# Performance work log

Measured on AMD Instinct MI355X. Metric: run time of the kernel, lower is better.

## Reference

```python
import jax, jax.numpy as jnp
import numpy as np

K = 10  # CSLS neighborhood size


def setup_inputs() -> dict:
    key = jax.random.key(0)
    k1, k2 = jax.random.split(key)
    N, D = 16384, 512
    Lvec = jax.random.normal(k1, (N, D), dtype=jnp.float32)
    Rvec = jax.random.normal(k2, (N, D), dtype=jnp.float32)
    return {"Lvec": Lvec, "Rvec": Rvec}


def reference(Lvec, Rvec):
    N = Lvec.shape[0]
    # L_sim[i, j] = <L_i, R_j>; R_sim = L_sim.T since both slices cover all rows
    sim = jnp.matmul(Lvec, Rvec.T)                      # [N_L, N_R]
    # CSLS penalties: mean of top-k similarities per row
    LR = jnp.mean(jax.lax.top_k(sim, K)[0], axis=-1)    # [N_L] per-L-entity top-k avg
    RL = jnp.mean(jax.lax.top_k(sim.T, K)[0], axis=-1)  # [N_R] per-R-entity top-k avg
    # Faithful to the torch epoch-0 broadcasting: both penalties broadcast over columns
    # csls[i, j] = 2 * R_sim[i, j] - LR[j] - RL[j]
    csls = 2.0 * sim.T - LR[None, :] - RL[None, :]      # [N_R, N_L]
    order = jnp.argsort(-csls, axis=-1)                 # descending rank lists
    # rank position of the true answer (column i for row i)
    ranks = jnp.argmax(order == jnp.arange(N)[:, None], axis=-1)  # [N] int
    top1_val = jnp.max(csls, axis=-1)                   # top-1 CSLS score per row
    return (ranks.astype(jnp.int32), top1_val)
```

## Files before the change

kernel.cpp:

```cpp
#include <hip/hip_runtime.h>
#include <hip/hip_bf16.h>
#include <hip/hip_fp8.h>
#include <stdint.h>

#define NN 16384
#define DD 512
#define BM 128
#define BN 256
#define NCT2 64
#define KT 6
#define EPW 264
#define NEG_INF (-3.0e38f)


typedef unsigned short u16;
typedef _Float16 f16;
typedef __attribute__((ext_vector_type(8))) __bf16 bf16x8;
typedef __attribute__((ext_vector_type(8))) short sh8;
typedef __attribute__((ext_vector_type(8))) _Float16 f16x8;
typedef __attribute__((ext_vector_type(4))) float f32x4;

__device__ __forceinline__ u16 f2bf(float f) {
  uint32_t x = __float_as_uint(f);
  x += 0x7fffu + ((x >> 16) & 1u);
  return (u16)(x >> 16);
}
__device__ __forceinline__ float bf2f(u16 u) {
  return __uint_as_float(((uint32_t)u) << 16);
}
__device__ __forceinline__ float f16bits(uint32_t bits) {
  f16 h;
  u16 b = (u16)bits;
  __builtin_memcpy(&h, &b, 2);
  return (float)h;
}
__device__ __forceinline__ u16 h2bits(f16 h) {
  u16 b;
  __builtin_memcpy(&b, &h, 2);
  return b;
}
__device__ __forceinline__ uint8_t f2fp8(float f) {
  __hip_fp8_e4m3 h(f);
  return (uint8_t)h.__x;
}
__device__ __forceinline__ float fp82f(uint8_t b) {
  __hip_fp8_e4m3 h;
  h.__x = (__hip_fp8_storage_t)b;
  return (float)h;
}
__device__ __forceinline__ uint32_t pk_max16(uint32_t a, uint32_t b) {
  uint32_t d;
  asm("v_pk_max_f16 %0, %1, %2" : "=v"(d) : "v"(a), "v"(b));
  return d;
}
__device__ __forceinline__ uint32_t pk_min16(uint32_t a, uint32_t b) {
  uint32_t d;
  asm("v_pk_min_f16 %0, %1, %2" : "=v"(d) : "v"(a), "v"(b));
  return d;
}

__device__ __forceinline__ void gload_lds16(const u16* g, u16* lds) {
  __builtin_amdgcn_global_load_lds(
      (const __attribute__((address_space(1))) uint32_t*)g,
      (__attribute__((address_space(3))) uint32_t*)lds,
      16, 0, 0);
}

template <int N>
__device__ __forceinline__ void insN(float (&t)[N], float v) {
  #pragma unroll
  for (int j = 0; j < N; ++j) {
    float hi = fmaxf(t[j], v);
    v = fminf(t[j], v);
    t[j] = hi;
  }
}
template <int N>
__device__ __forceinline__ void pinsN(uint32_t (&t)[N], uint32_t v) {
  #pragma unroll
  for (int j = 0; j < N; ++j) {
    uint32_t hi = pk_max16(t[j], v);
    v = pk_min16(t[j], v);
    t[j] = hi;
  }
}

__global__ __launch_bounds__(256) void cast_kernel(const float* __restrict__ src,
                                                   u16* __restrict__ dst) {
  int i = (blockIdx.x * 256 + threadIdx.x) * 8;
  const float4* s4 = reinterpret_cast<const float4*>(src + i);
  float4 a = s4[0], b = s4[1];
  sh8 o;
  o[0] = (short)f2bf(a.x); o[1] = (short)f2bf(a.y);
  o[2] = (short)f2bf(a.z); o[3] = (short)f2bf(a.w);
  o[4] = (short)f2bf(b.x); o[5] = (short)f2bf(b.y);
  o[6] = (short)f2bf(b.z); o[7] = (short)f2bf(b.w);
  *reinterpret_cast<sh8*>(dst + i) = o;
}

__global__ __launch_bounds__(256) void diag_kernel(const u16* __restrict__ Lb,
                                                   const u16* __restrict__ Rb,
                                                   float* __restrict__ diag) {
  int r = blockIdx.x * 4 + (threadIdx.x >> 6);
  int lane = threadIdx.x & 63;
  sh8 a = *reinterpret_cast<const sh8*>(Lb + (size_t)r * DD + lane * 8);
  sh8 b = *reinterpret_cast<const sh8*>(Rb + (size_t)r * DD + lane * 8);
  float s = 0.f;
  #pragma unroll
  for (int j = 0; j < 8; ++j) s += bf2f((u16)a[j]) * bf2f((u16)b[j]);
  #pragma unroll
  for (int off = 32; off > 0; off >>= 1) s += __shfl_down(s, off);
  if (lane == 0) diag[r] = s;
}

#define DECODE_TILE(ct0)                                \
  const int xcd = blockIdx.x & 7;                       \
  const int idx = blockIdx.x >> 3;                      \
  const int rowtile = xcd * 16 + (idx & 15);            \
  const int coltile = (ct0) + (idx >> 4);               \
  const int rowbase = rowtile * BM;                     \
  const int colbase = coltile * BN;                     \
  const int tid = threadIdx.x;                          \
  const int w = tid >> 6;                               \
  const int lane = tid & 63;                            \
  const int quad = lane >> 4;                           \
  const int l16 = lane & 15;                            \
  const int wr = (w >> 2) * 64;                         \
  const int wc = (w & 3) * 64;                          \
  (void)xcd; (void)lane;

#define GEMM_PRE()                                                              \
  const int rp0_ = tid >> 3, gp0_ = (tid & 7) ^ (rp0_ & 7);                     \
  const int grow0_ = rp0_ * 2 + (gp0_ >> 2), gcol0_ = (gp0_ & 3) * 8;           \
  const int gl1_ = tid + 512;                                                   \
  const int rp1_ = gl1_ >> 3, gp1_ = (gl1_ & 7) ^ (rp1_ & 7);                   \
  const int grow1_ = rp1_ * 2 + (gp1_ >> 2), gcol1_ = (gp1_ & 3) * 8;           \
  const u16* gA_  = A + (size_t)(rowbase + grow0_) * DD + gcol0_;               \
  const u16* gB0_ = B + (size_t)(colbase + grow0_) * DD + gcol0_;               \
  const u16* gB1_ = B + (size_t)(colbase + grow1_) * DD + gcol1_;               \
  const int gsel_ = ((((l16) & 1) << 2) + quad) ^ (l16 >> 1);                   \
  const int rdA_ = (wr / 2 + (l16 >> 1)) * 64 + gsel_ * 8;                      \
  const int rdB_ = (wc / 2 + (l16 >> 1)) * 64 + gsel_ * 8;

#define STAGE(t, dA, dB)                                                        \
  gload_lds16(gA_  + (t) * 32, (dA) + tid * 8);                                 \
  gload_lds16(gB0_ + (t) * 32, (dB) + tid * 8);                                 \
  gload_lds16(gB1_ + (t) * 32, (dB) + 4096 + tid * 8);

#define GEMM_K_LOOP(sA0_, sA1_, sB0_, sB1_)                                     \
  f32x4 acc[4][4];                                                              \
  _Pragma("unroll")                                                             \
  for (int a_ = 0; a_ < 4; ++a_)                                                \
    _Pragma("unroll")                                                           \
    for (int b_ = 0; b_ < 4; ++b_) acc[a_][b_] = (f32x4){0.f, 0.f, 0.f, 0.f};   \
  {                                                                             \
    GEMM_PRE()                                                                  \
    u16* const bufA_[2] = {(sA0_), (sA1_)};                                     \
    u16* const bufB_[2] = {(sB0_), (sB1_)};                                     \
    STAGE(0, bufA_[0], bufB_[0])                                                \
    STAGE(1, bufA_[1], bufB_[1])                                                \
    _Pragma("unroll")                                                           \
    for (int t = 0; t < 16; ++t) {                                              \
      if (t < 15) { asm volatile("s_waitcnt vmcnt(3)" ::: "memory"); }          \
      else        { asm volatile("s_waitcnt vmcnt(0)" ::: "memory"); }          \
      __builtin_amdgcn_s_barrier();                                             \
      asm volatile("" ::: "memory");                                            \
      {                                                                         \
        const u16* cA_ = bufA_[t & 1];                                          \
        const u16* cB_ = bufB_[t & 1];                                          \
        bf16x8 af[4], bfv[4];                                                   \
        _Pragma("unroll")                                                       \
        for (int f = 0; f < 4; ++f)                                             \
          af[f]  = *reinterpret_cast<const bf16x8*>(cA_ + rdA_ + f * 512);      \
        _Pragma("unroll")                                                       \
        for (int f = 0; f < 4; ++f)                                             \
          bfv[f] = *reinterpret_cast<const bf16x8*>(cB_ + rdB_ + f * 512);      \
        _Pragma("unroll")                                                       \
        for (int fr = 0; fr < 4; ++fr)                                          \
          _Pragma("unroll")                                                     \
          for (int fc = 0; fc < 4; ++fc)                                        \
            acc[fr][fc] = __builtin_amdgcn_mfma_f32_16x16x32_bf16(af[fr], bfv[fc], acc[fr][fc], 0, 0, 0); \
      }                                                                         \
      asm volatile("" ::: "memory");                                            \
      __builtin_amdgcn_s_barrier();                                             \
      if (t + 2 < 16) { STAGE(t + 2, bufA_[t & 1], bufB_[t & 1]) }              \
    }                                                                           \
  }

__global__ __launch_bounds__(512, 4) void gemm_topk(const u16* __restrict__ A,
                                                    const u16* __restrict__ B,
                                                    f16* __restrict__ rowp,
                                                    f16* __restrict__ colp,
                                                    uint8_t* __restrict__ sim,
                                                    int SC2) {
  __shared__ __align__(16) u16 smem[33792];
  u16* sA0 = smem;
  u16* sA1 = smem + 4096;
  u16* sB0 = smem + 8192;
  u16* sB1 = smem + 16384;
  DECODE_TILE(0)
  GEMM_K_LOOP(sA0, sA1, sB0, sB1)

  f16* hC = reinterpret_cast<f16*>(smem);
  #pragma unroll
  for (int fr = 0; fr < 4; ++fr)
    #pragma unroll
    for (int fc = 0; fc < 4; ++fc)
      #pragma unroll
      for (int reg = 0; reg < 4; ++reg)
        hC[(wr + 16 * fr + quad * 4 + reg) * EPW + wc + 16 * fc + l16] =
            (f16)acc[fr][fc][reg];
  __syncthreads();
  if (coltile < SC2) {
    const int SW = SC2 * BN;
    uint8_t* gs = sim + (size_t)rowbase * SW + (size_t)coltile * BN;
    #pragma unroll
    for (int itw = 0; itw < 8; ++itw) {
      int idx2 = itw * 4096 + tid * 8;
      int rr = idx2 >> 8, cc = idx2 & 255;
      f16x8 v = *reinterpret_cast<const f16x8*>(hC + rr * EPW + cc);
      uint32_t lo = 0, hi = 0;
      #pragma unroll
      for (int j = 0; j < 4; ++j) lo |= (uint32_t)f2fp8((float)v[j]) << (8 * j);
      #pragma unroll
      for (int j = 0; j < 4; ++j) hi |= (uint32_t)f2fp8((float)v[4 + j]) << (8 * j);
      uint2 o;
      o.x = lo; o.y = hi;
      *reinterpret_cast<uint2*>(gs + (size_t)rr * SW + cc) = o;
    }
  }
  uint32_t trow[KT];
  #pragma unroll
  for (int j = 0; j < KT; ++j) trow[j] = 0xFBFFFBFFu;
  {
    const u16* q = reinterpret_cast<const u16*>(hC) + (tid >> 2) * EPW + (tid & 3) * 64;
    #pragma unroll
    for (int c8 = 0; c8 < 8; ++c8) {
      uint4 ch = *reinterpret_cast<const uint4*>(q + c8 * 8);
      pinsN<KT>(trow, ch.x);
      pinsN<KT>(trow, ch.y);
      pinsN<KT>(trow, ch.z);
      pinsN<KT>(trow, ch.w);
    }
  }
  uint32_t tcol[KT];
  #pragma unroll
  for (int j = 0; j < KT; ++j) tcol[j] = 0xFBFFFBFFu;
  const int cp = tid & 127, rq = tid >> 7;
  {
    const u16* base = reinterpret_cast<const u16*>(hC) + rq * 32 * EPW + 2 * cp;
    #pragma unroll 8
    for (int i = 0; i < 32; ++i) {
      uint32_t v = *reinterpret_cast<const uint32_t*>(base + i * EPW);
      pinsN<KT>(tcol, v);
    }
  }
  __syncthreads();
  uint32_t* sCl = reinterpret_cast<uint32_t*>(smem);
  uint32_t* sRl = reinterpret_cast<uint32_t*>(smem) + 128 * 4 * KT;
  #pragma unroll
  for (int j = 0; j < KT; ++j) sCl[(cp * 4 + rq) * KT + j] = tcol[j];
  #pragma unroll
  for (int j = 0; j < KT; ++j) sRl[tid * KT + j] = trow[j];
  __syncthreads();
  if (tid < 256) {
    float best[KT];
    #pragma unroll
    for (int j = 0; j < KT; ++j) best[j] = NEG_INF;
    const int cpp = tid >> 1, par = tid & 1;
    for (int rqi = 0; rqi < 4; ++rqi)
      for (int j = 0; j < KT; ++j) {
        uint32_t u = sCl[(cpp * 4 + rqi) * KT + j];
        float v = f16bits(par ? (u >> 16) : u);
        if (v > best[KT - 1]) insN<KT>(best, v);
        else break;
      }
    f16* o = colp + ((size_t)rowtile * NN + colbase + tid) * KT;
    uint32_t w0 = h2bits((f16)best[0]) | ((uint32_t)h2bits((f16)best[1]) << 16);
    uint32_t w1 = h2bits((f16)best[2]) | ((uint32_t)h2bits((f16)best[3]) << 16);
    uint32_t w2 = h2bits((f16)best[4]) | ((uint32_t)h2bits((f16)best[5]) << 16);
    uint32_t* o32 = reinterpret_cast<uint32_t*>(o);
    o32[0] = w0; o32[1] = w1; o32[2] = w2;
  } else if (tid < 384) {
    const int r = tid - 256;
    float best[KT];
    #pragma unroll
    for (int j = 0; j < KT; ++j) best[j] = NEG_INF;
    for (int h = 0; h < 4; ++h)
      for (int par = 0; par < 2; ++par)
        for (int j = 0; j < KT; ++j) {
          uint32_t u = sRl[(r * 4 + h) * KT + j];
          float v = f16bits(par ? (u >> 16) : u);
          if (v > best[KT - 1]) insN<KT>(best, v);
          else break;
        }
    f16* o = rowp + ((size_t)coltile * NN + rowbase + r) * KT;
    uint32_t w0 = h2bits((f16)best[0]) | ((uint32_t)h2bits((f16)best[1]) << 16);
    uint32_t w1 = h2bits((f16)best[2]) | ((uint32_t)h2bits((f16)best[3]) << 16);
    uint32_t w2 = h2bits((f16)best[4]) | ((uint32_t)h2bits((f16)best[5]) << 16);
    uint32_t* o32 = reinterpret_cast<uint32_t*>(o);
    o32[0] = w0; o32[1] = w1; o32[2] = w2;
  }
}

__global__ __launch_bounds__(512, 4) void gemm_rank(const u16* __restrict__ A,
                                                    const u16* __restrict__ B,
                                                    const float* __restrict__ p,
                                                    const float* __restrict__ thr,
                                                    int* __restrict__ cnt_out,
                                                    float* __restrict__ mx_out,
                                                    int ct0) {
  __shared__ __align__(16) u16 smem[24576];
  u16* sA0 = smem;
  u16* sA1 = smem + 4096;
  u16* sB0 = smem + 8192;
  u16* sB1 = smem + 16384;
  DECODE_TILE(ct0)

  GEMM_K_LOOP(sA0, sA1, sB0, sB1)

  float thrv[16];
  #pragma unroll
  for (int i = 0; i < 16; ++i)
    thrv[i] = thr[rowbase + wr + 16 * (i >> 2) + quad * 4 + (i & 3)];
  float pv[4];
  #pragma unroll
  for (int fc = 0; fc < 4; ++fc) pv[fc] = p[colbase + wc + 16 * fc + l16];

  int cnt[16];
  float mx[16];
  #pragma unroll
  for (int i = 0; i < 16; ++i) { cnt[i] = 0; mx[i] = NEG_INF; }
  #pragma unroll
  for (int fc = 0; fc < 4; ++fc)
    #pragma unroll
    for (int fr = 0; fr < 4; ++fr)
      #pragma unroll
      for (int reg = 0; reg < 4; ++reg) {
        float t2 = 2.f * acc[fr][fc][reg] - pv[fc];
        int idx2 = fr * 4 + reg;
        cnt[idx2] += (t2 > thrv[idx2]) ? 1 : 0;
        mx[idx2] = fmaxf(mx[idx2], t2);
      }

  float* sMx = reinterpret_cast<float*>(smem);
  int*   sCn = reinterpret_cast<int*>(smem) + 512;
  #pragma unroll
  for (int idx2 = 0; idx2 < 16; ++idx2) {
    int c = cnt[idx2];
    float m = mx[idx2];
    #pragma unroll
    for (int off = 1; off < 16; off <<= 1) {
      c += __shfl_xor(c, off);
      m = fmaxf(m, __shfl_xor(m, off));
    }
    if (l16 == 0) {
      int rloc = 16 * (idx2 >> 2) + quad * 4 + (idx2 & 3);
      sMx[w * 64 + rloc] = m;
      sCn[w * 64 + rloc] = c;
    }
  }
  __syncthreads();
  if (tid < 128) {
    int g0 = (tid >> 6) * 4, rloc = tid & 63;
    int c = 0;
    float m = NEG_INF;
    #pragma unroll
    for (int k = 0; k < 4; ++k) {
      c += sCn[(g0 + k) * 64 + rloc];
      m = fmaxf(m, sMx[(g0 + k) * 64 + rloc]);
    }
    cnt_out[(size_t)coltile * NN + rowbase + tid] = c;
    mx_out[(size_t)coltile * NN + rowbase + tid] = m;
  }
}

__global__ __launch_bounds__(256) void scan_kernel(const uint8_t* __restrict__ sim,
                                                   const float* __restrict__ p,
                                                   const float* __restrict__ thr,
                                                   int SC2,
                                                   int* __restrict__ cnt_s,
                                                   float* __restrict__ mx_s) {
  const int tid = threadIdx.x;
  const int row0 = blockIdx.x * 4;
  const int SW = SC2 * BN;
  float t[4];
  #pragma unroll
  for (int r = 0; r < 4; ++r) t[r] = thr[row0 + r];
  int cnt[4] = {0, 0, 0, 0};
  float m[4] = {NEG_INF, NEG_INF, NEG_INF, NEG_INF};
  for (int c0 = tid * 16; c0 < SW; c0 += 4096) {
    float pv[16];
    {
      const float4* p4 = reinterpret_cast<const float4*>(p + c0);
      *reinterpret_cast<float4*>(&pv[0])  = p4[0];
      *reinterpret_cast<float4*>(&pv[4])  = p4[1];
      *reinterpret_cast<float4*>(&pv[8])  = p4[2];
      *reinterpret_cast<float4*>(&pv[12]) = p4[3];
    }
    #pragma unroll
    for (int r = 0; r < 4; ++r) {
      uint4 v = *reinterpret_cast<const uint4*>(sim + (size_t)(row0 + r) * SW + c0);
      uint32_t wds[4] = {v.x, v.y, v.z, v.w};
      #pragma unroll
      for (int j = 0; j < 16; ++j) {
        float sv = fp82f((uint8_t)(wds[j >> 2] >> ((j & 3) * 8)));
        float t2 = 2.f * sv - pv[j];
        cnt[r] += (t2 > t[r]) ? 1 : 0;
        m[r] = fmaxf(m[r], t2);
      }
    }
  }
  __shared__ float sM[4][4];
  __shared__ int sC[4][4];
  const int lane = tid & 63, w = tid >> 6;
  #pragma unroll
  for (int r = 0; r < 4; ++r) {
    int c = cnt[r];
    float mm = m[r];
    #pragma unroll
    for (int off = 32; off > 0; off >>= 1) {
      c += __shfl_down(c, off);
      mm = fmaxf(mm, __shfl_down(mm, off));
    }
    if (lane == 0) { sC[r][w] = c; sM[r][w] = mm; }
  }
  __syncthreads();
  if (tid < 4) {
    int c = sC[tid][0] + sC[tid][1] + sC[tid][2] + sC[tid][3];
    float mm = fmaxf(fmaxf(sM[tid][0], sM[tid][1]), fmaxf(sM[tid][2], sM[tid][3]));
    cnt_s[row0 + tid] = c;
    mx_s[row0 + tid] = mm;
  }
}

__global__ __launch_bounds__(256) void p_kernel(const f16* __restrict__ rowp,
                                                const f16* __restrict__ colp,
                                                const float* __restrict__ diag,
                                                float* __restrict__ pout,
                                                float* __restrict__ throut) {
  __shared__ float sB1[64][4][10];
  __shared__ float sB2[64][4][10];
  const int tid = threadIdx.x;
  const int lent = tid >> 2, part = tid & 3;
  const int l = blockIdx.x * 64 + lent;
  float b1[10], b2[10];
  #pragma unroll
  for (int j = 0; j < 10; ++j) { b1[j] = NEG_INF; b2[j] = NEG_INF; }
  for (int s = part * 16; s < part * 16 + 16; ++s) {
    const uint32_t* q1 = reinterpret_cast<const uint32_t*>(rowp + ((size_t)s * NN + l) * KT);
    #pragma unroll
    for (int d = 0; d < 3; ++d) {
      uint32_t u = q1[d];
      float v0 = f16bits(u), v1 = f16bits(u >> 16);
      if (v0 > b1[9]) insN<10>(b1, v0); else break;
      if (v1 > b1[9]) insN<10>(b1, v1); else break;
    }
  }
  for (int s = part * 32; s < part * 32 + 32; ++s) {
    const uint32_t* q2 = reinterpret_cast<const uint32_t*>(colp + ((size_t)s * NN + l) * KT);
    #pragma unroll
    for (int d = 0; d < 3; ++d) {
      uint32_t u = q2[d];
      float v0 = f16bits(u), v1 = f16bits(u >> 16);
      if (v0 > b2[9]) insN<10>(b2, v0); else break;
      if (v1 > b2[9]) insN<10>(b2, v1); else break;
    }
  }
  #pragma unroll
  for (int j = 0; j < 10; ++j) { sB1[lent][part][j] = b1[j]; sB2[lent][part][j] = b2[j]; }
  __syncthreads();
  if (tid < 64) {
    const int l2 = blockIdx.x * 64 + tid;
    float m1[10], m2[10];
    #pragma unroll
    for (int j = 0; j < 10; ++j) { m1[j] = NEG_INF; m2[j] = NEG_INF; }
    for (int pa = 0; pa < 4; ++pa) {
      for (int j = 0; j < 10; ++j) {
        float v = sB1[tid][pa][j];
        if (v > m1[9]) insN<10>(m1, v); else break;
      }
      for (int j = 0; j < 10; ++j) {
        float v = sB2[tid][pa][j];
        if (v > m2[9]) insN<10>(m2, v); else break;
      }
    }
    float s1 = 0.f, s2 = 0.f;
    #pragma unroll
    for (int j = 0; j < 10; ++j) { s1 += m1[j]; s2 += m2[j]; }
    float pv = (s1 + s2) * 0.1f;
    pout[l2] = pv;
    throut[l2] = 2.f * diag[l2] - pv;
  }
}

__global__ __launch_bounds__(256) void final_kernel(const int* __restrict__ cnt,
                                                    const float* __restrict__ mx,
                                                    const int* __restrict__ cnt_s,
                                                    const float* __restrict__ mx_s,
                                                    int sc2,
                                                    float* __restrict__ out) {
  int r = blockIdx.x * 256 + threadIdx.x;
  int c = 0;
  float m = NEG_INF;
  if (sc2 > 0) { c = cnt_s[r]; m = mx_s[r]; }
  for (int s = sc2; s < NCT2; ++s) {
    c += cnt[(size_t)s * NN + r];
    m = fmaxf(m, mx[(size_t)s * NN + r]);
  }
  out[r] = (float)c;
  out[NN + r] = m;
}

extern "C" void kernel_launch(void* const* d_in, const int* in_sizes, int n_in,
                              void* d_out, int out_size, void* d_ws, size_t ws_size,
                              hipStream_t stream) {
  const float* L = (const float*)d_in[0];
  const float* R = (const float*)d_in[1];
  char* ws = (char*)d_ws;

  const size_t PART_ROW = (size_t)NCT2 * NN * KT * 2;
  const size_t PART_COL = (size_t)128 * NN * KT * 2;
  const size_t TAILOFF = (32ull << 20) + PART_ROW + PART_COL;
  const size_t SIMOFF = TAILOFF + (320ull << 10);

  u16* Lb   = (u16*)ws;
  u16* Rb   = (u16*)(ws + (16ull << 20));
  f16* rowp = (f16*)(ws + (32ull << 20));
  f16* colp = (f16*)(ws + (32ull << 20) + PART_ROW);
  char* tail = ws + TAILOFF;
  float* diag   = (float*)tail;
  float* pbuf   = (float*)(tail + (64ull << 10));
  float* thrbuf = (float*)(tail + (128ull << 10));
  int*   cnt_s  = (int*)(tail + (192ull << 10));
  float* mx_s   = (float*)(tail + (256ull << 10));
  uint8_t* sim  = (uint8_t*)(ws + SIMOFF);
  int*   cntp = (int*)rowp;
  float* mxp  = (float*)colp;

  int SC2 = 0;
  if (ws_size > SIMOFF) {
    size_t sc = (ws_size - SIMOFF) / ((size_t)NN * BN * 1);
    if (sc > 64) sc = 64;
    SC2 = (int)sc;
  }

  cast_kernel<<<(NN * DD / (256 * 8)), 256, 0, stream>>>(L, Lb);
  cast_kernel<<<(NN * DD / (256 * 8)), 256, 0, stream>>>(R, Rb);
  diag_kernel<<<NN / 4, 256, 0, stream>>>(Lb, Rb, diag);
  gemm_topk<<<(NN / BM) * NCT2, 512, 0, stream>>>(Rb, Lb, rowp, colp, sim, SC2);
  p_kernel<<<NN / 64, 256, 0, stream>>>(rowp, colp, diag, pbuf, thrbuf);
  if (SC2 > 0)
    scan_kernel<<<NN / 4, 256, 0, stream>>>(sim, pbuf, thrbuf, SC2, cnt_s, mx_s);
  if (SC2 < NCT2)
    gemm_rank<<<(NN / BM) * (NCT2 - SC2), 512, 0, stream>>>(Rb, Lb, pbuf, thrbuf,
                                                            cntp, mxp, SC2);
  final_kernel<<<NN / 256, 256, 0, stream>>>(cntp, mxp, cnt_s, mx_s, SC2,
                                             (float*)d_out);
}
```

Before: 649.1 us.

## Keep top-4 per tile partial lists and pack fp8 with hardware converts

Cuts each tile's partial top-k list for rows and columns from 6 to 4 candidates. The partial lists can then be written and read as single 8-byte vector accesses, and insertion work and memory traffic for the partials shrink. The fp8 packing of the similarity matrix now uses the cvt_pk_fp8_f32 builtin when it exists instead of converting one element at a time. Keeping only 4 per tile risks losing true top-10 members when more than 4 of a row's top-10 fall in the same tile, which changes the CSLS penalties.

Result: faster. 580.6 us (-10.6%).

```diff
diff --git a/kernel.cpp b/kernel.cpp
--- a/kernel.cpp
+++ b/kernel.cpp
@@ -8,7 +8,7 @@
 #define BM 128
 #define BN 256
 #define NCT2 64
-#define KT 6
+#define KT 4
 #define EPW 264
 #define NEG_INF (-3.0e38f)
 
@@ -47,6 +47,16 @@
   __hip_fp8_e4m3 h;
   h.__x = (__hip_fp8_storage_t)b;
   return (float)h;
+}
+__device__ __forceinline__ uint32_t pk4_fp8(float a, float b, float c, float d) {
+#if defined(__has_builtin) && __has_builtin(__builtin_amdgcn_cvt_pk_fp8_f32)
+  int v = __builtin_amdgcn_cvt_pk_fp8_f32(a, b, 0, false);
+  v = __builtin_amdgcn_cvt_pk_fp8_f32(c, d, v, true);
+  return (uint32_t)v;
+#else
+  return (uint32_t)f2fp8(a) | ((uint32_t)f2fp8(b) << 8) |
+         ((uint32_t)f2fp8(c) << 16) | ((uint32_t)f2fp8(d) << 24);
+#endif
 }
 __device__ __forceinline__ uint32_t pk_max16(uint32_t a, uint32_t b) {
   uint32_t d;
@@ -219,13 +229,9 @@
       int idx2 = itw * 4096 + tid * 8;
       int rr = idx2 >> 8, cc = idx2 & 255;
       f16x8 v = *reinterpret_cast<const f16x8*>(hC + rr * EPW + cc);
-      uint32_t lo = 0, hi = 0;
-      #pragma unroll
-      for (int j = 0; j < 4; ++j) lo |= (uint32_t)f2fp8((float)v[j]) << (8 * j);
-      #pragma unroll
-      for (int j = 0; j < 4; ++j) hi |= (uint32_t)f2fp8((float)v[4 + j]) << (8 * j);
       uint2 o;
-      o.x = lo; o.y = hi;
+      o.x = pk4_fp8((float)v[0], (float)v[1], (float)v[2], (float)v[3]);
+      o.y = pk4_fp8((float)v[4], (float)v[5], (float)v[6], (float)v[7]);
       *reinterpret_cast<uint2*>(gs + (size_t)rr * SW + cc) = o;
     }
   }
@@ -276,11 +282,10 @@
         else break;
       }
     f16* o = colp + ((size_t)rowtile * NN + colbase + tid) * KT;
-    uint32_t w0 = h2bits((f16)best[0]) | ((uint32_t)h2bits((f16)best[1]) << 16);
-    uint32_t w1 = h2bits((f16)best[2]) | ((uint32_t)h2bits((f16)best[3]) << 16);
-    uint32_t w2 = h2bits((f16)best[4]) | ((uint32_t)h2bits((f16)best[5]) << 16);
-    uint32_t* o32 = reinterpret_cast<uint32_t*>(o);
-    o32[0] = w0; o32[1] = w1; o32[2] = w2;
+    uint2 ov;
+    ov.x = h2bits((f16)best[0]) | ((uint32_t)h2bits((f16)best[1]) << 16);
+    ov.y = h2bits((f16)best[2]) | ((uint32_t)h2bits((f16)best[3]) << 16);
+    *reinterpret_cast<uint2*>(o) = ov;
   } else if (tid < 384) {
     const int r = tid - 256;
     float best[KT];
@@ -295,11 +300,10 @@
           else break;
         }
     f16* o = rowp + ((size_t)coltile * NN + rowbase + r) * KT;
-    uint32_t w0 = h2bits((f16)best[0]) | ((uint32_t)h2bits((f16)best[1]) << 16);
-    uint32_t w1 = h2bits((f16)best[2]) | ((uint32_t)h2bits((f16)best[3]) << 16);
-    uint32_t w2 = h2bits((f16)best[4]) | ((uint32_t)h2bits((f16)best[5]) << 16);
-    uint32_t* o32 = reinterpret_cast<uint32_t*>(o);
-    o32[0] = w0; o32[1] = w1; o32[2] = w2;
+    uint2 ov;
+    ov.x = h2bits((f16)best[0]) | ((uint32_t)h2bits((f16)best[1]) << 16);
+    ov.y = h2bits((f16)best[2]) | ((uint32_t)h2bits((f16)best[3]) << 16);
+    *reinterpret_cast<uint2*>(o) = ov;
   }
 }
 
@@ -448,20 +452,22 @@
   #pragma unroll
   for (int j = 0; j < 10; ++j) { b1[j] = NEG_INF; b2[j] = NEG_INF; }
   for (int s = part * 16; s < part * 16 + 16; ++s) {
-    const uint32_t* q1 = reinterpret_cast<const uint32_t*>(rowp + ((size_t)s * NN + l) * KT);
-    #pragma unroll
-    for (int d = 0; d < 3; ++d) {
-      uint32_t u = q1[d];
+    uint2 u2 = *reinterpret_cast<const uint2*>(rowp + ((size_t)s * NN + l) * KT);
+    uint32_t ud[2] = {u2.x, u2.y};
+    #pragma unroll
+    for (int d = 0; d < 2; ++d) {
+      uint32_t u = ud[d];
       float v0 = f16bits(u), v1 = f16bits(u >> 16);
       if (v0 > b1[9]) insN<10>(b1, v0); else break;
       if (v1 > b1[9]) insN<10>(b1, v1); else break;
     }
   }
   for (int s = part * 32; s < part * 32 + 32; ++s) {
-    const uint32_t* q2 = reinterpret_cast<const uint32_t*>(colp + ((size_t)s * NN + l) * KT);
-    #pragma unroll
-    for (int d = 0; d < 3; ++d) {
-      uint32_t u = q2[d];
+    uint2 u2 = *reinterpret_cast<const uint2*>(colp + ((size_t)s * NN + l) * KT);
+    uint32_t ud[2] = {u2.x, u2.y};
+    #pragma unroll
+    for (int d = 0; d < 2; ++d) {
+      uint32_t u = ud[d];
       float v0 = f16bits(u), v1 = f16bits(u >> 16);
       if (v0 > b2[9]) insN<10>(b2, v0); else break;
       if (v1 > b2[9]) insN<10>(b2, v1); else break;
```
